# Performance work log

Measured on AMD Instinct MI355X. Metric: run time of the kernel, lower is better.

Reference implementation:

```python
import jax, jax.numpy as jnp
import numpy as np

N = 100000      # points
K = 16          # neighbors (nsample)
C_IN = 128      # d_in
C_OUT = 256     # d_out
NK = 15         # kernel points (k_015)
SIGMA = 0.3
SCALE = SIGMA ** 2 * 2 + 1e-10
BN_EPS = 1e-5


def setup_inputs() -> dict:
    key = jax.random.key(0)
    ks = jax.random.split(key, 6)
    p = jax.random.normal(ks[0], (N, 3), dtype=jnp.float32)
    x = jax.random.normal(ks[1], (N, C_IN), dtype=jnp.float32)
    idx = jax.random.randint(ks[2], (N, K), 0, N, dtype=jnp.int32)
    kernel_point = jax.random.normal(ks[3], (1, NK, 3), dtype=jnp.float32) * 0.5
    conv_w = jax.random.normal(ks[4], (C_OUT, C_IN + 3, NK), dtype=jnp.float32) * 0.02
    conv_b = jax.random.normal(ks[5], (C_OUT,), dtype=jnp.float32) * 0.02
    bn_gamma = jnp.ones((C_OUT,), dtype=jnp.float32)
    bn_beta = jnp.zeros((C_OUT,), dtype=jnp.float32)
    bn_mean = jnp.zeros((C_OUT,), dtype=jnp.float32)
    bn_var = jnp.ones((C_OUT,), dtype=jnp.float32)
    return {"p": p, "x": x, "kernel_point": kernel_point, "conv_w": conv_w,
            "conv_b": conv_b, "bn_gamma": bn_gamma, "bn_beta": bn_beta,
            "bn_mean": bn_mean, "bn_var": bn_var, "idx": idx}


def reference(p, x, kernel_point, conv_w, conv_b, bn_gamma, bn_beta, bn_mean, bn_var, idx):
    # --- queryandgroup (use_xyz=True), neighbor indices precomputed ---
    pj = p[idx] - p[:, None, :]        # [N, K, 3] relative coords
    xj = x[idx]                        # [N, K, C_IN]
    # --- DepthwiseKPConv (first_layer branch: d_in != d_out) ---
    l2 = jnp.linalg.norm(pj, axis=2, keepdims=True)               # [N, K, 1]
    pj = pj / (jnp.max(l2, axis=1, keepdims=True) + 1e-10)        # normalize by max neighbor dist
    diff = kernel_point[:, :, None, :] - pj[:, None, :, :]        # [N, NK, K, 3]
    corr = jnp.exp(-jnp.sum(diff * diff, axis=-1) / SCALE)        # [N, NK, K]
    xj = jnp.concatenate([pj, xj], axis=-1)                       # [N, K, C_IN+3]
    agg = jnp.einsum('nmk,nkc->nmc', corr, xj)                    # [N, NK, C_IN+3]
    # Conv1d(C_IN+3, C_OUT, kernel=NK): full contraction over channel & kernel axes
    y = jnp.einsum('nmc,ocm->no', agg, conv_w) + conv_b           # [N, C_OUT]
    # BatchNorm1d (eval stats) + ReLU
    y = (y - bn_mean) * (bn_gamma / jnp.sqrt(bn_var + BN_EPS)) + bn_beta
    return jax.nn.relu(y)
```

## Files before the change

kernel.cpp:

```cpp
#include <hip/hip_runtime.h>
#include <hip/hip_fp16.h>

#define N_PTS   100000
#define KNB     16
#define CIN     128
#define COUT    256
#define NKP     15
#define CCH     131
#define KP      2112
#define MPAD    100096
#define CHROWS  50048

typedef _Float16 f16x8 __attribute__((ext_vector_type(8)));
typedef float    f32x4 __attribute__((ext_vector_type(4)));
typedef unsigned int u32x2 __attribute__((ext_vector_type(2)));

__device__ __forceinline__ void g2lds16(const void* g, void* l) {
  __builtin_amdgcn_global_load_lds((const __attribute__((address_space(1))) void*)g,
                                   (__attribute__((address_space(3))) void*)l, 16, 0, 0);
}

__global__ __launch_bounds__(256) void k_prep_x(const float* __restrict__ x,
                                                __half* __restrict__ xh) {
  int i = blockIdx.x * 256 + threadIdx.x;
  float4 v = ((const float4*)x)[i];
  __half2* o = (__half2*)xh;
  o[i * 2]     = __floats2half2_rn(v.x, v.y);
  o[i * 2 + 1] = __floats2half2_rn(v.z, v.w);
}

__global__ __launch_bounds__(256) void k_prep_w(
    const float* __restrict__ w, const float* __restrict__ cb,
    const float* __restrict__ g, const float* __restrict__ be,
    const float* __restrict__ mu, const float* __restrict__ var,
    __half* __restrict__ wt, float* __restrict__ sc, float* __restrict__ sh) {
  int gid = blockIdx.x * 256 + threadIdx.x;
  int o = gid / KP, r = gid - o * KP;
  int c = r >> 4, m = r & 15;
  float v = 0.f;
  if (m < 15 && c < 131) {
    int refch = (c < 128) ? (8 * (c & 15) + (c >> 4) + 3) : (c - 128);
    v = w[(o * CCH + refch) * NKP + m];
  }
  wt[gid] = __float2half(v);
  if (gid < COUT) {
    float s = g[gid] / sqrtf(var[gid] + 1e-5f);
    sc[gid] = s;
    sh[gid] = (cb[gid] - mu[gid]) * s + be[gid];
  }
}

__global__ __launch_bounds__(256) void k_agg(
    const float* __restrict__ p, const __half* __restrict__ xh,
    const float* __restrict__ kp, const int* __restrict__ idx,
    __half* __restrict__ agg, int r0) {
  __shared__ float pj[4][16][4];
  __shared__ float co[4][16][16];
  const int l = threadIdx.x & 63;
  const int w = threadIdx.x >> 6;
  const int n = r0 + blockIdx.x * 4 + w;
  const int nc = (n < N_PTS) ? n : (N_PTS - 1);
  const int cfix = l & 15;
  const int nbr = idx[nc * KNB + cfix];

  int rowoff[8];
  #pragma unroll
  for (int i = 0; i < 8; i++)
    rowoff[i] = __shfl(nbr, ((l >> 4) & 1) * 8 + i) * (CIN * 2);

  const char* xb = (const char*)xh + cfix * 16;
  f16x8 xq[8];
  #pragma unroll
  for (int i = 0; i < 8; i++)
    xq[i] = *(const f16x8*)(xb + (size_t)(unsigned)rowoff[i]);

  const float cx = p[nc * 3], cy = p[nc * 3 + 1], cz = p[nc * 3 + 2];
  float ax = p[nbr * 3]     - cx;
  float ay = p[nbr * 3 + 1] - cy;
  float az = p[nbr * 3 + 2] - cz;
  float mx = sqrtf(ax * ax + ay * ay + az * az);
  #pragma unroll
  for (int d = 1; d < 16; d <<= 1) mx = fmaxf(mx, __shfl_xor(mx, d));
  const float inv = 1.0f / (mx + 1e-10f);
  ax *= inv; ay *= inv; az *= inv;

  if (l < 16) { pj[w][l][0] = ax; pj[w][l][1] = ay; pj[w][l][2] = az; pj[w][l][3] = 0.f; }
  __syncthreads();

  const int k1 = l >> 2;
  f32x4 pv = *(const f32x4*)&pj[w][k1][0];
  f32x4 cc;
  #pragma unroll
  for (int j = 0; j < 4; j++) {
    int m = (l & 3) * 4 + j;
    if (m < 15) {
      float dx = kp[m * 3] - pv[0], dy = kp[m * 3 + 1] - pv[1], dz = kp[m * 3 + 2] - pv[2];
      cc[j] = __expf((dx * dx + dy * dy + dz * dz) * -5.5555553f);
    } else cc[j] = 0.f;
  }
  *(f32x4*)&co[w][k1][(l & 3) * 4] = cc;
  __syncthreads();

  f16x8 af = {};
  if (l < 32) {
    #pragma unroll
    for (int i = 0; i < 8; i++)
      af[i] = (_Float16)co[w][(l >> 4) * 8 + i][l & 15];
  }

  const bool live = (n < N_PTS);
  const int g4 = (l >> 4) * 4;
  char* outp = (char*)(agg + (size_t)(n - r0) * KP) + cfix * 32 + g4 * 2;

  #pragma unroll
  for (int g = 0; g < 8; g++) {
    f16x8 bf;
    #pragma unroll
    for (int i = 0; i < 8; i++)
      bf[i] = xq[i][g];
    f32x4 d = __builtin_amdgcn_mfma_f32_16x16x32_f16(af, bf, (f32x4){0.f, 0.f, 0.f, 0.f}, 0, 0, 0);
    if (live) {
      __half2 h0 = __floats2half2_rn(d[0], d[1]);
      __half2 h1 = __floats2half2_rn(d[2], d[3]);
      u32x2 u; u.x = *(unsigned int*)&h0; u.y = *(unsigned int*)&h1;
      *(u32x2*)(outp + g * 512) = u;
    }
  }
  {
    f16x8 bf = {};
    if (l < 32 && cfix < 3) {
      #pragma unroll
      for (int i = 0; i < 8; i++)
        bf[i] = (_Float16)pj[w][(l >> 4) * 8 + i][cfix];
    }
    f32x4 d = __builtin_amdgcn_mfma_f32_16x16x32_f16(af, bf, (f32x4){0.f, 0.f, 0.f, 0.f}, 0, 0, 0);
    if (live && cfix < 4) {
      __half2 h0 = __floats2half2_rn(d[0], d[1]);
      __half2 h1 = __floats2half2_rn(d[2], d[3]);
      u32x2 u; u.x = *(unsigned int*)&h0; u.y = *(unsigned int*)&h1;
      *(u32x2*)(outp + 8 * 512) = u;
    }
  }
}

__global__ __launch_bounds__(256) void k_gemm(
    const __half* __restrict__ A, const __half* __restrict__ B,
    const float* __restrict__ sc, const float* __restrict__ sh,
    float* __restrict__ out, int r0) {
  __shared__ __align__(16) __half Al[128 * 64];
  __shared__ __align__(16) __half Bl[128 * 64];
  const int t = threadIdx.x;
  const int l = t & 63;
  const int bn = blockIdx.x, bm = blockIdx.y;
  const int m0 = bm * 128, n0 = bn * 128;
  const int w = t >> 6;
  const int wm = w >> 1, wn = w & 1;

  f32x4 acc[4][4] = {};

  const int arow = t >> 3;
  const int kb   = (t & 7) << 4;
  const int kbsw = kb ^ ((arow & 7) << 4);
  const char* aSrc = (const char*)(A + (size_t)(m0 + arow) * KP) + kbsw;
  const char* bSrc = (const char*)(B + (size_t)(n0 + arow) * KP) + kbsw;
  char* aDst = (char*)Al + t * 16;
  char* bDst = (char*)Bl + t * 16;
  const size_t rowStride32 = (size_t)32 * KP * 2;

  for (int kt = 0; kt < KP / 64; kt++) {
    __syncthreads();
    #pragma unroll
    for (int i = 0; i < 4; i++) {
      g2lds16(aSrc + i * rowStride32 + (size_t)kt * 128, aDst + i * 4096);
      g2lds16(bSrc + i * rowStride32 + (size_t)kt * 128, bDst + i * 4096);
    }
    __syncthreads();
    #pragma unroll
    for (int kk = 0; kk < 2; kk++) {
      f16x8 af[4], bf[4];
      const int rbyte = ((l >> 4) << 4) + kk * 64;
      #pragma unroll
      for (int i = 0; i < 4; i++) {
        const int ra = wm * 64 + i * 16 + (l & 15);
        af[i] = *(const f16x8*)((const char*)Al + ra * 128 + (rbyte ^ ((ra & 7) << 4)));
        const int rb = wn * 64 + i * 16 + (l & 15);
        bf[i] = *(const f16x8*)((const char*)Bl + rb * 128 + (rbyte ^ ((rb & 7) << 4)));
      }
      #pragma unroll
      for (int i = 0; i < 4; i++)
        #pragma unroll
        for (int j = 0; j < 4; j++)
          acc[i][j] = __builtin_amdgcn_mfma_f32_16x16x32_f16(af[i], bf[j], acc[i][j], 0, 0, 0);
    }
  }

  #pragma unroll
  for (int j = 0; j < 4; j++) {
    const int col = n0 + wn * 64 + j * 16 + (l & 15);
    const float s = sc[col], h = sh[col];
    #pragma unroll
    for (int i = 0; i < 4; i++) {
      const int rr = r0 + m0 + wm * 64 + i * 16 + ((l >> 4) << 2);
      #pragma unroll
      for (int rg = 0; rg < 4; rg++) {
        const int r = rr + rg;
        if (r < N_PTS) {
          float v = acc[i][j][rg] * s + h;
          out[(size_t)r * COUT + col] = fmaxf(v, 0.f);
        }
      }
    }
  }
}

extern "C" void kernel_launch(void* const* d_in, const int* in_sizes, int n_in,
                              void* d_out, int out_size, void* d_ws, size_t ws_size,
                              hipStream_t stream) {
  (void)in_sizes; (void)n_in; (void)out_size;
  const float* p   = (const float*)d_in[0];
  const float* x   = (const float*)d_in[1];
  const float* kp  = (const float*)d_in[2];
  const float* w   = (const float*)d_in[3];
  const float* cb  = (const float*)d_in[4];
  const float* g   = (const float*)d_in[5];
  const float* be  = (const float*)d_in[6];
  const float* mu  = (const float*)d_in[7];
  const float* var = (const float*)d_in[8];
  const int* idx   = (const int*)d_in[9];
  float* out = (float*)d_out;

  char* ws = (char*)d_ws;
  size_t off = 0;
  __half* wt  = (__half*)(ws + off); off += (size_t)COUT * KP * 2;
  float*  sc  = (float*)(ws + off);  off += 1024;
  float*  sh  = (float*)(ws + off);  off += 1024;
  __half* xh  = (__half*)(ws + off); off += (size_t)N_PTS * CIN * 2;
  __half* agg = (__half*)(ws + off);
  size_t avail = (ws_size > off) ? (ws_size - off) : 0;

  size_t maxrows = avail / ((size_t)KP * 2);
  int rows = CHROWS;
  if (maxrows < (size_t)rows) rows = (int)(maxrows & ~(size_t)127);
  if (rows < 128) rows = 128;

  hipLaunchKernelGGL(k_prep_x, dim3(N_PTS * CIN / 1024), dim3(256), 0, stream, x, xh);
  hipLaunchKernelGGL(k_prep_w, dim3(COUT * KP / 256), dim3(256), 0, stream,
                     w, cb, g, be, mu, var, wt, sc, sh);

  for (int row0 = 0; row0 < N_PTS; row0 += rows) {
    int rr = MPAD - row0;
    if (rr > rows) rr = rows;
    hipLaunchKernelGGL(k_agg, dim3(rr / 4), dim3(256), 0, stream, p, xh, kp, idx, agg, row0);
    hipLaunchKernelGGL(k_gemm, dim3(2, rr / 128), dim3(256), 0, stream, agg, wt, sc, sh, out, row0);
  }
}
```

Before: 556.9 us.

## Double-buffer LDS tiles in GEMM to overlap global loads with MFMA

Makes the A and B shared-memory tiles double-buffered. The next K-tile is issued with global_load_lds into the alternate buffer before computing on the current one. Explicit vmcnt/lgkmcnt waits and s_barrier replace the two __syncthreads per iteration, so load latency can hide behind MFMA work. This doubles LDS use per block (64KB), which may cut occupancy, and it depends on hand-counted vmcnt values being correct.

```diff
diff --git a/kernel.cpp b/kernel.cpp
--- a/kernel.cpp
+++ b/kernel.cpp
@@ -147,8 +147,8 @@
     const __half* __restrict__ A, const __half* __restrict__ B,
     const float* __restrict__ sc, const float* __restrict__ sh,
     float* __restrict__ out, int r0) {
-  __shared__ __align__(16) __half Al[128 * 64];
-  __shared__ __align__(16) __half Bl[128 * 64];
+  __shared__ __align__(16) __half Al[2][128 * 64];
+  __shared__ __align__(16) __half Bl[2][128 * 64];
   const int t = threadIdx.x;
   const int l = t & 63;
   const int bn = blockIdx.x, bm = blockIdx.y;
@@ -163,18 +163,32 @@
   const int kbsw = kb ^ ((arow & 7) << 4);
   const char* aSrc = (const char*)(A + (size_t)(m0 + arow) * KP) + kbsw;
   const char* bSrc = (const char*)(B + (size_t)(n0 + arow) * KP) + kbsw;
-  char* aDst = (char*)Al + t * 16;
-  char* bDst = (char*)Bl + t * 16;
   const size_t rowStride32 = (size_t)32 * KP * 2;
 
-  for (int kt = 0; kt < KP / 64; kt++) {
-    __syncthreads();
-    #pragma unroll
-    for (int i = 0; i < 4; i++) {
-      g2lds16(aSrc + i * rowStride32 + (size_t)kt * 128, aDst + i * 4096);
-      g2lds16(bSrc + i * rowStride32 + (size_t)kt * 128, bDst + i * 4096);
-    }
-    __syncthreads();
+  #define STAGE(BUF, KT) { _Pragma("unroll") for (int i = 0; i < 4; i++) {            \
+      g2lds16(aSrc + i * rowStride32 + (size_t)(KT) * 128,                            \
+              (char*)Al + (BUF) * 16384 + t * 16 + i * 4096);                         \
+      g2lds16(bSrc + i * rowStride32 + (size_t)(KT) * 128,                            \
+              (char*)Bl + (BUF) * 16384 + t * 16 + i * 4096); } }
+
+  const int NT = KP / 64;
+  STAGE(0, 0)
+  __builtin_amdgcn_sched_barrier(0);
+
+  for (int kt = 0; kt < NT; kt++) {
+    const int cur = kt & 1;
+    if (kt + 1 < NT) {
+      STAGE(cur ^ 1, kt + 1)
+      __builtin_amdgcn_sched_barrier(0);
+      asm volatile("s_waitcnt vmcnt(8)" ::: "memory");
+    } else {
+      asm volatile("s_waitcnt vmcnt(0)" ::: "memory");
+    }
+    __builtin_amdgcn_s_barrier();
+    __builtin_amdgcn_sched_barrier(0);
+
+    const char* Ab = (const char*)Al + cur * 16384;
+    const char* Bb = (const char*)Bl + cur * 16384;
     #pragma unroll
     for (int kk = 0; kk < 2; kk++) {
       f16x8 af[4], bf[4];
@@ -182,9 +196,9 @@
       #pragma unroll
       for (int i = 0; i < 4; i++) {
         const int ra = wm * 64 + i * 16 + (l & 15);
-        af[i] = *(const f16x8*)((const char*)Al + ra * 128 + (rbyte ^ ((ra & 7) << 4)));
+        af[i] = *(const f16x8*)(Ab + ra * 128 + (rbyte ^ ((ra & 7) << 4)));
         const int rb = wn * 64 + i * 16 + (l & 15);
-        bf[i] = *(const f16x8*)((const char*)Bl + rb * 128 + (rbyte ^ ((rb & 7) << 4)));
+        bf[i] = *(const f16x8*)(Bb + rb * 128 + (rbyte ^ ((rb & 7) << 4)));
       }
       #pragma unroll
       for (int i = 0; i < 4; i++)
@@ -192,7 +206,12 @@
         for (int j = 0; j < 4; j++)
           acc[i][j] = __builtin_amdgcn_mfma_f32_16x16x32_f16(af[i], bf[j], acc[i][j], 0, 0, 0);
     }
-  }
+
+    asm volatile("s_waitcnt lgkmcnt(0)" ::: "memory");
+    __builtin_amdgcn_s_barrier();
+    __builtin_amdgcn_sched_barrier(0);
+  }
+  #undef STAGE
 
   #pragma unroll
   for (int j = 0; j < 4; j++) {
```

New measurement: 519.0 us. -6.8%, faster.
